# Kernel optimization log

Hardware: AMD Instinct MI355X
Metric: run time of the kernel (lower is better)

## Reference

```python
import jax, jax.numpy as jnp
import numpy as np
import math

# Mamba2Simple(d_model=192, d_state=128, d_conv=4, expand=4, headdim=32, chunk_size=256)
D_MODEL = 192
D_STATE = 128
D_CONV = 4
EXPAND = 4
HEADDIM = 32
D_INNER = EXPAND * D_MODEL                      # 768
NHEADS = D_INNER // HEADDIM                     # 24
CONV_DIM = D_INNER + 2 * D_STATE                # 1024 (ngroups=1)
D_IN_PROJ = 2 * D_INNER + 2 * D_STATE + NHEADS  # 1816
SEQ_PAD = 256                                   # forward pads dim-2 to 256
NUM_CLASS = 100
FEATURE_DIM = HEADDIM * D_STATE                 # 4096, classifier input


def make_pe(max_len, d_model):
    # TemporalPositionalEncoding buffer (sin/cos), added over the T axis.
    position = np.arange(max_len)[:, None].astype(np.float32)
    div_term = np.exp(np.arange(0, d_model, 2).astype(np.float32) * -(math.log(10000.0) / d_model))
    pe = np.zeros((max_len, d_model), np.float32)
    pe[:, 0::2] = np.sin(position * div_term)
    pe[:, 1::2] = np.cos(position * div_term)
    return jnp.asarray(pe)  # (max_len, d_model)


def setup_inputs() -> dict:
    key = jax.random.key(0)
    ks = jax.random.split(key, 8)
    B, T, S, D = 16, 8, 129, D_MODEL
    inputs = jax.random.normal(ks[0], (B, T, S, D), jnp.float32)
    in_proj_w = jax.random.normal(ks[1], (D_IN_PROJ, D_MODEL), jnp.float32) / np.sqrt(D_MODEL)
    conv_w = jax.random.normal(ks[2], (CONV_DIM, D_CONV), jnp.float32) / np.sqrt(D_CONV)
    conv_b = jax.random.normal(ks[3], (CONV_DIM,), jnp.float32) * 0.1
    # dt_bias = softplus^{-1}(dt) with dt ~ U[1e-3, 0.1] (Mamba2 init convention)
    dt0 = jax.random.uniform(ks[4], (NHEADS,), jnp.float32, 1e-3, 0.1)
    dt_bias = jnp.log(jnp.expm1(dt0))
    A_log = jnp.log(jax.random.uniform(ks[5], (NHEADS,), jnp.float32, 1.0, 16.0))
    cls_w = jax.random.normal(ks[6], (NUM_CLASS, FEATURE_DIM), jnp.float32) / np.sqrt(FEATURE_DIM)
    cls_b = jnp.zeros((NUM_CLASS,), jnp.float32)
    return dict(inputs=inputs, in_proj_w=in_proj_w, conv_w=conv_w, conv_b=conv_b,
                dt_bias=dt_bias, A_log=A_log, cls_w=cls_w, cls_b=cls_b)


def _mamba_final_state(u, in_proj_w, conv_w, conv_b, dt_bias, A_log):
    # u: (B, L, D_MODEL). Only the SSM final state is consumed downstream
    # (the module does `_, final_state = self.mamba(...)`), so the z / C / D /
    # RMSNormGated / out_proj branches, which never touch the state, are skipped.
    B_, L, _ = u.shape
    W = in_proj_w[D_INNER:, :]                              # rows for xBC (1024) + dt (24)
    proj = jnp.einsum('bld,ed->ble', u, W)                  # (B, L, 1048)
    xBC, dt_raw = proj[..., :CONV_DIM], proj[..., CONV_DIM:]
    # causal depthwise conv1d (kernel D_CONV) + SiLU
    xpad = jnp.pad(xBC, ((0, 0), (D_CONV - 1, 0), (0, 0)))
    conv = conv_b + sum(xpad[:, k:k + L, :] * conv_w[:, k] for k in range(D_CONV))
    xBC = jax.nn.silu(conv)
    x = xBC[..., :D_INNER].reshape(B_, L, NHEADS, HEADDIM)  # (B, L, H, P)
    Bmat = xBC[..., D_INNER:D_INNER + D_STATE]              # (B, L, N), ngroups=1
    dt = jax.nn.softplus(dt_raw + dt_bias)                  # (B, L, H)
    A = -jnp.exp(A_log)                                     # (H,), negative
    # Recurrence: h_t = exp(dt_t*A) * h_{t-1} + dt_t * x_t (outer) B_t.
    # Final state in closed form via exclusive suffix products of exp(dt*A):
    logdA = dt * A                                          # (B, L, H), <= 0
    csum = jnp.cumsum(logdA, axis=1)
    suffix = jnp.exp(csum[:, -1:, :] - csum)                # prod_{s>t} exp(dt_s*A)
    w = suffix * dt                                         # (B, L, H)
    return jnp.einsum('blh,blhp,bln->bhpn', w, x, Bmat)     # (B, H, P, N)


def reference(inputs, in_proj_w, conv_w, conv_b, dt_bias, A_log, cls_w, cls_b):
    # Dropout layers are identity in eval mode.
    B_, T, S, D = inputs.shape
    x = inputs[:, :, 1:, :]                                 # drop first sub-seq element
    pad = SEQ_PAD - x.shape[2]
    if pad > 0:
        x = jnp.pad(x, ((0, 0), (0, 0), (0, pad), (0, 0)))
    pe = make_pe(T, D)
    x = x + pe[None, :, None, :]                            # pe broadcast over batch & sub-seq
    preds = []
    for t in range(T):                                      # module re-runs scan on each suffix
        xt = x[:, t:, :, :].reshape(B_, -1, D)              # (B, (T-t)*256, D)
        h = _mamba_final_state(xt, in_proj_w, conv_w, conv_b, dt_bias, A_log)
        agg = h.sum(axis=1).reshape(B_, FEATURE_DIM)        # sum over heads -> (B, P*N)
        preds.append(agg @ cls_w.T + cls_b)
    return jnp.stack(preds, axis=1)                         # (B, T, NUM_CLASS)
```

## Files before the change

### kernel.cpp

```cpp
#include <hip/hip_runtime.h>
#include <math.h>

#define BATCH 16
#define TWIN 8
#define SEQIN 129
#define DMODEL 192
#define GLEN 2048
#define NH 24
#define HD 32
#define DS 128
#define NCC 896
#define MTOT (BATCH*GLEN)
#define NVALID (BATCH*TWIN*128)
#define PADK 40

typedef __attribute__((ext_vector_type(8))) short bf16x8;
typedef __attribute__((ext_vector_type(4))) float f32x4;

__device__ __forceinline__ float softplus_f(float x){
  return x > 20.f ? x : log1pf(expf(x));
}
__device__ __forceinline__ float silu_f(float x){
  return x / (1.f + __expf(-x));
}
__device__ __forceinline__ unsigned short tobf16(float f){
  union { float f; unsigned u; } v; v.f = f;
  unsigned r = v.u + 0x7FFF + ((v.u >> 16) & 1);
  return (unsigned short)(r >> 16);
}
__device__ __forceinline__ float frombf16(unsigned short u){
  union { unsigned u; float f; } v; v.u = ((unsigned)u) << 16; return v.f;
}
__device__ __forceinline__ bf16x8 pack8(float4 a, float4 b){
  bf16x8 r;
  r[0]=(short)tobf16(a.x); r[1]=(short)tobf16(a.y);
  r[2]=(short)tobf16(a.z); r[3]=(short)tobf16(a.w);
  r[4]=(short)tobf16(b.x); r[5]=(short)tobf16(b.y);
  r[6]=(short)tobf16(b.z); r[7]=(short)tobf16(b.w);
  return r;
}

__global__ __launch_bounds__(256) void k_build(const float* __restrict__ in,
    const float* __restrict__ inw, unsigned short* __restrict__ inh,
    unsigned short* __restrict__ wh, float* __restrict__ ptab,
    float* __restrict__ dtraw){
  __shared__ float smem[2048];
  int bx = blockIdx.x;
  int tid = threadIdx.x;
  if (bx < 768){
    int idx = (bx*256 + tid)*16;
    int v = idx / DMODEL;
    int d = idx - v*DMODEL;
    int bt = v >> 7, s = v & 127;
    const float* src = in + ((size_t)bt*SEQIN + s + 1)*DMODEL + d;
    float4 a0 = *(const float4*)src;
    float4 a1 = *(const float4*)(src+4);
    float4 a2 = *(const float4*)(src+8);
    float4 a3 = *(const float4*)(src+12);
    *(bf16x8*)&inh[idx]   = pack8(a0, a1);
    *(bf16x8*)&inh[idx+8] = pack8(a2, a3);
  } else if (bx < 852){
    int idx = ((bx-768)*256 + tid)*8;
    const float* src = inw + (size_t)768*DMODEL + idx;
    float4 a = *(const float4*)src;
    float4 b = *(const float4*)(src+4);
    *(bf16x8*)&wh[idx] = pack8(a, b);
  } else if (bx < 916){
    float* pe = smem;
    int pb = bx - 852;
    int t = pb >> 3, eslice = pb & 7;
    if (tid < DMODEL){
      int d = tid;
      float div = expf(-(float)(d & ~1) * (logf(10000.f)/(float)DMODEL));
      float ang = (float)t * div;
      pe[d] = (d & 1) ? cosf(ang) : sinf(ang);
    }
    __syncthreads();
    int e0 = eslice*115;
    int e1 = min(920, e0 + 115);
    for (int e = e0 + tid; e < e1; e += 256){
      int row = (e < 896) ? (768 + e) : (1792 + (e - 896));
      const float* wr = inw + (size_t)row*DMODEL;
      float s = 0.f;
      #pragma unroll 4
      for (int d = 0; d < DMODEL; d++)
        s += pe[d] * wr[d];
      ptab[t*920 + e] = s;
    }
  } else {
    float* As = smem;
    float* Bs = smem + 1024;
    int idx = bx - 916;
    int m0 = idx*64;
    int bt = m0 >> 7, srow = m0 & 127;
    int ty = tid >> 4, tx = tid & 15;
    int lr = tid >> 2, lq = tid & 3;
    float acc[4][4] = {};
    for (int k0 = 0; k0 < DMODEL; k0 += 16){
      float4 av = *(const float4*)(in + ((size_t)bt*SEQIN + srow + 1 + lr)*DMODEL + k0 + lq*4);
      As[(lq*4+0)*64+lr] = av.x; As[(lq*4+1)*64+lr] = av.y;
      As[(lq*4+2)*64+lr] = av.z; As[(lq*4+3)*64+lr] = av.w;
      float4 bv = make_float4(0.f,0.f,0.f,0.f);
      if (lr < NH) bv = *(const float4*)(inw + (size_t)(1792+lr)*DMODEL + k0 + lq*4);
      Bs[(lq*4+0)*64+lr] = bv.x; Bs[(lq*4+1)*64+lr] = bv.y;
      Bs[(lq*4+2)*64+lr] = bv.z; Bs[(lq*4+3)*64+lr] = bv.w;
      __syncthreads();
      #pragma unroll
      for (int kk = 0; kk < 16; kk++){
        float4 a = *(const float4*)&As[kk*64 + ty*4];
        float4 bq = *(const float4*)&Bs[kk*64 + tx*4];
        float avr[4] = {a.x, a.y, a.z, a.w};
        float bvr[4] = {bq.x, bq.y, bq.z, bq.w};
        #pragma unroll
        for (int i=0;i<4;i++)
          #pragma unroll
          for (int j=0;j<4;j++)
            acc[i][j] += avr[i]*bvr[j];
      }
      __syncthreads();
    }
    #pragma unroll
    for (int i=0;i<4;i++){
      int m = m0 + ty*4 + i;
      #pragma unroll
      for (int j=0;j<4;j++){
        int n = tx*4 + j;
        if (n < NH) dtraw[(size_t)m*NH + n] = acc[i][j];
      }
    }
  }
}

__global__ __launch_bounds__(256) void k_gemmall(const unsigned short* __restrict__ inh,
    const unsigned short* __restrict__ wh, const float* __restrict__ ptab,
    const float* __restrict__ dtraw, const float* __restrict__ dt_bias,
    const float* __restrict__ A_log, unsigned short* __restrict__ projh,
    float* __restrict__ wbuf, float* __restrict__ wsum){
  __shared__ char smem[20480];
  int bx = blockIdx.x;
  int tid = threadIdx.x;
  if (bx < 896){
    unsigned short* As = (unsigned short*)smem;
    unsigned short* Bs = As + 128*PADK;
    int mt = bx & 127;
    int n0 = (bx >> 7)*128;
    int t = mt & 7;
    size_t msrc = (size_t)mt*128;
    size_t mdst = (size_t)(mt >> 3)*GLEN + (size_t)t*256;
    int wid = tid >> 6, lane = tid & 63;
    int wm = (wid >> 1)*64, wn = (wid & 1)*64;
    int quad = lane >> 4, lm = lane & 15;
    int sr = tid >> 2, sq = tid & 3;
    f32x4 acc[4][4];
    #pragma unroll
    for (int i=0;i<4;i++)
      #pragma unroll
      for (int j=0;j<4;j++) acc[i][j] = (f32x4){0.f,0.f,0.f,0.f};
    for (int k0 = 0; k0 < DMODEL; k0 += 32){
      #pragma unroll
      for (int half=0; half<2; half++){
        int r = sr + half*64;
        *(bf16x8*)&As[r*PADK + sq*8] =
          *(const bf16x8*)&inh[(msrc + r)*DMODEL + k0 + sq*8];
        *(bf16x8*)&Bs[r*PADK + sq*8] =
          *(const bf16x8*)&wh[(size_t)(n0+r)*DMODEL + k0 + sq*8];
      }
      __syncthreads();
      bf16x8 aF[4], bF[4];
      #pragma unroll
      for (int i=0;i<4;i++){
        aF[i] = *(const bf16x8*)&As[(wm + i*16 + lm)*PADK + quad*8];
        bF[i] = *(const bf16x8*)&Bs[(wn + i*16 + lm)*PADK + quad*8];
      }
      #pragma unroll
      for (int i=0;i<4;i++)
        #pragma unroll
        for (int j=0;j<4;j++)
          acc[i][j] = __builtin_amdgcn_mfma_f32_16x16x32_bf16(aF[i], bF[j], acc[i][j], 0,0,0);
      __syncthreads();
    }
    float ptn[4];
    #pragma unroll
    for (int j=0;j<4;j++) ptn[j] = ptab[t*920 + n0 + wn + lm + j*16];
    #pragma unroll
    for (int i=0;i<4;i++){
      #pragma unroll
      for (int r=0;r<4;r++){
        int m = wm + i*16 + quad*4 + r;
        unsigned short* dst = projh + (mdst + m)*NCC + n0 + wn + lm;
        #pragma unroll
        for (int j=0;j<4;j++)
          dst[j*16] = tobf16(acc[i][j][r] + ptn[j]);
      }
    }
  } else if (bx < 1024){
    float* pt = (float*)smem;
    int bt = bx - 896;
    int b = bt >> 3, t = bt & 7;
    for (int e = tid; e < NCC; e += 256) pt[e] = ptab[t*920 + e];
    __syncthreads();
    size_t base = (size_t)b*GLEN + t*256;
    for (int i = tid; i < 12*224; i += 256){
      int r = i / 224, c4 = (i - r*224)*4;
      int s = (r < 8) ? (128 + r) : (244 + r);
      ushort4 v;
      v.x = tobf16(pt[c4+0]); v.y = tobf16(pt[c4+1]);
      v.z = tobf16(pt[c4+2]); v.w = tobf16(pt[c4+3]);
      *(ushort4*)&projh[(base + s)*NCC + c4] = v;
    }
  } else {
    float* wtot = (float*)smem;
    float* sred = (float*)smem + 4;
    int idx = bx - 1024;
    int h = idx % NH, b = idx / NH;
    int lane = tid & 63, wid = tid >> 6;
    int tw = tid >> 5, q = tid & 31;
    float dtb = dt_bias[h];
    float negA = -expf(A_log[h]);
    float off = ptab[tw*920 + 896 + h] + dtb;
    float dtv[8], pre[8];
    float run = 0.f;
    if (q < 16){
      size_t rb = ((size_t)(b*TWIN + tw)*128 + q*8)*NH + h;
      #pragma unroll
      for (int i=0;i<8;i++){
        float dt = softplus_f(dtraw[rb + (size_t)i*NH] + off);
        run += dt * negA;
        dtv[i] = dt; pre[i] = run;
      }
    } else {
      float dt = softplus_f(off);
      #pragma unroll
      for (int i=0;i<8;i++){
        run += dt * negA;
        dtv[i] = dt; pre[i] = run;
      }
    }
    float v = run;
    #pragma unroll
    for (int o=1; o<64; o<<=1){
      float u = __shfl_up(v, o, 64);
      if (lane >= o) v += u;
    }
    if (lane == 63) wtot[wid] = v;
    __syncthreads();
    float base = 0.f, total = 0.f;
    #pragma unroll
    for (int w2=0; w2<4; w2++){
      float tv = wtot[w2];
      if (w2 < wid) base += tv;
      total += tv;
    }
    float excl = base + v - run;
    float ls = 0.f;
    size_t gb = (size_t)b*GLEN + tw*256 + q*8;
    #pragma unroll
    for (int i=0;i<8;i++){
      float w = expf(total - (excl + pre[i])) * dtv[i];
      if (q < 17) wbuf[(gb + i)*NH + h] = w;
      else ls += w;
    }
    sred[tid] = ls;
    __syncthreads();
    if (q == 17){
      float acc = ls;
      for (int r = 18; r < 32; r++) acc += sred[tw*32 + r];
      wsum[((size_t)b*TWIN + tw)*NH + h] = acc;
    }
  }
}

__global__ __launch_bounds__(256) void k_foldall(const unsigned short* __restrict__ projh,
    const float* __restrict__ conv_w, const float* __restrict__ conv_b,
    const float* __restrict__ wbuf, const float* __restrict__ ptab,
    const float* __restrict__ wsum, float* __restrict__ partial,
    float* __restrict__ cB, float* __restrict__ cbuf){
  __shared__ float smem[5440];
  int bx = blockIdx.x;
  int tid = threadIdx.x;
  if (bx < 512){
    int bt = bx >> 2, sub = bx & 3;
    int b = bt >> 3, t = bt & 7;
    int wave = tid >> 6, lane = tid & 63;
    int g0 = t*256 + sub*34;
    int wstart = wave*8 + (wave > 0 ? 1 : 0);
    int gw = g0 + wstart;
    size_t rbase = (size_t)b*GLEN;
    float* ybuf = smem;
    float cb[7][2], cw[7][2][4];
    #pragma unroll
    for (int k=0;k<7;k++){
      int c = 2*lane + 128*k;
      float2 tb = *(const float2*)&conv_b[c];
      cb[k][0]=tb.x; cb[k][1]=tb.y;
      float4 w0 = *(const float4*)&conv_w[c*4];
      float4 w1 = *(const float4*)&conv_w[(c+1)*4];
      cw[k][0][0]=w0.x; cw[k][0][1]=w0.y; cw[k][0][2]=w0.z; cw[k][0][3]=w0.w;
      cw[k][1][0]=w1.x; cw[k][1][1]=w1.y; cw[k][1][2]=w1.z; cw[k][1][3]=w1.w;
    }
    float h0[7][2], h1[7][2], h2[7][2];
    #pragma unroll
    for (int k=0;k<7;k++){
      h0[k][0]=h0[k][1]=h1[k][0]=h1[k][1]=h2[k][0]=h2[k][1]=0.f;
    }
    if (gw >= 3){
      #pragma unroll
      for (int k=0;k<7;k++){
        int c = 2*lane + 128*k;
        ushort2 p0 = *(const ushort2*)&projh[(rbase+gw-3)*NCC + c];
        ushort2 p1 = *(const ushort2*)&projh[(rbase+gw-2)*NCC + c];
        ushort2 p2 = *(const ushort2*)&projh[(rbase+gw-1)*NCC + c];
        h0[k][0]=frombf16(p0.x); h0[k][1]=frombf16(p0.y);
        h1[k][0]=frombf16(p1.x); h1[k][1]=frombf16(p1.y);
        h2[k][0]=frombf16(p2.x); h2[k][1]=frombf16(p2.y);
      }
    }
    #pragma unroll
    for (int i=0;i<9;i++){
      size_t row = rbase + gw + i;
      float wreg = (lane < NH) ? wbuf[row*NH + lane] : 0.f;
      float cur[7][2];
      #pragma unroll
      for (int k=0;k<7;k++){
        int c = 2*lane + 128*k;
        ushort2 pv = *(const ushort2*)&projh[row*NCC + c];
        cur[k][0]=frombf16(pv.x); cur[k][1]=frombf16(pv.y);
      }
      float py0=0.f, py1=0.f, b0v=0.f, b1v=0.f;
      #pragma unroll
      for (int k=0;k<7;k++){
        float a0 = cb[k][0] + h0[k][0]*cw[k][0][0] + h1[k][0]*cw[k][0][1]
                            + h2[k][0]*cw[k][0][2] + cur[k][0]*cw[k][0][3];
        float a1 = cb[k][1] + h0[k][1]*cw[k][1][0] + h1[k][1]*cw[k][1][1]
                            + h2[k][1]*cw[k][1][2] + cur[k][1]*cw[k][1][3];
        float s0 = silu_f(a0), s1 = silu_f(a1);
        if (k < 6){
          float wh_ = __shfl(wreg, (lane>>4) + 4*k, 64);
          py0 += wh_*s0; py1 += wh_*s1;
        } else { b0v = s0; b1v = s1; }
      }
      py0 += __shfl_xor(py0, 16, 64); py0 += __shfl_xor(py0, 32, 64);
      py1 += __shfl_xor(py1, 16, 64); py1 += __shfl_xor(py1, 32, 64);
      float* dst = ybuf + (wstart + i)*160;
      if (lane < 16) *(float2*)&dst[2*lane] = make_float2(py0, py1);
      *(float2*)&dst[32 + 2*lane] = make_float2(b0v, b1v);
      #pragma unroll
      for (int k=0;k<7;k++){
        h0[k][0]=h1[k][0]; h0[k][1]=h1[k][1];
        h1[k][0]=h2[k][0]; h1[k][1]=h2[k][1];
        h2[k][0]=cur[k][0]; h2[k][1]=cur[k][1];
      }
    }
    __syncthreads();
    int p0 = (tid >> 5)*4, n0 = (tid & 31)*4;
    float acc[4][4] = {};
    #pragma unroll 2
    for (int gi = 0; gi < 34; gi++){
      float4 yv = *(const float4*)&ybuf[gi*160 + p0];
      float4 bv = *(const float4*)&ybuf[gi*160 + 32 + n0];
      float ya[4] = {yv.x,yv.y,yv.z,yv.w};
      float ba[4] = {bv.x,bv.y,bv.z,bv.w};
      #pragma unroll
      for (int i=0;i<4;i++)
        #pragma unroll
        for (int j=0;j<4;j++)
          acc[i][j] += ya[i]*ba[j];
    }
    size_t pb = ((size_t)bt*4 + sub)*4096;
    #pragma unroll
    for (int i=0;i<4;i++)
      #pragma unroll
      for (int j=0;j<4;j++)
        partial[pb + (p0+i)*128 + n0+j] = acc[i][j];
  } else if (bx < 640){
    float* Xc = smem;
    float* Ws = smem + 896;
    int idx = bx - 512;
    int t = idx & 7, b = idx >> 3;
    for (int c = tid; c < NCC; c += 256){
      float4 w = *(const float4*)&conv_w[c*4];
      float sw = w.x + w.y + w.z + w.w;
      float a = conv_b[c] + frombf16(tobf16(ptab[t*920 + c])) * sw;
      Xc[c] = silu_f(a);
    }
    if (tid < NH) Ws[tid] = wsum[((size_t)b*TWIN + t)*NH + tid];
    __syncthreads();
    float* dst = cB + ((size_t)(b*TWIN + t))*160;
    if (tid < 32){
      float y = 0.f;
      #pragma unroll
      for (int h=0;h<NH;h++) y += Ws[h]*Xc[h*32 + tid];
      dst[tid] = y;
    } else if (tid < 160){
      dst[tid] = Xc[768 + tid - 32];
    }
  } else {
    float* xsw  = smem;
    float* xsg  = smem + 896;
    float* wv   = smem + 1792;
    float* bufw = smem + 1816;
    float* bufg = smem + 2296;
    int idx = bx - 640;
    int b = idx / 7, t = idx % 7 + 1;
    size_t rbase = (size_t)b*GLEN;
    int g0 = t*256;
    for (int gi=0; gi<3; gi++){
      int g = g0 + gi;
      if (tid < NH) wv[tid] = wbuf[(rbase+g)*NH + tid];
      for (int c = tid; c < NCC; c += 256){
        float aw = conv_b[c], ag = conv_b[c];
        #pragma unroll
        for (int k=0;k<4;k++){
          int gp = g - 3 + k;
          float term = frombf16(projh[(rbase+gp)*NCC + c]) * conv_w[c*4+k];
          ag += term;
          if (gp >= g0) aw += term;
        }
        xsw[c] = silu_f(aw);
        xsg[c] = silu_f(ag);
      }
      __syncthreads();
      if (tid < 32){
        float yw = 0.f, yg = 0.f;
        #pragma unroll
        for (int h=0;h<NH;h++){ yw += wv[h]*xsw[h*32+tid]; yg += wv[h]*xsg[h*32+tid]; }
        bufw[gi*160 + tid] = yw;
        bufg[gi*160 + tid] = yg;
      } else if (tid < 160){
        bufw[gi*160 + tid] = xsw[768 + tid - 32];
        bufg[gi*160 + tid] = xsg[768 + tid - 32];
      }
      __syncthreads();
    }
    float* dst = cbuf + ((size_t)(b*TWIN + t))*960;
    for (int i = tid; i < 960; i += 256){
      int gi = i / 320, rem = i - gi*320;
      dst[i] = (rem < 160) ? bufw[gi*160 + rem] : bufg[gi*160 + rem - 160];
    }
  }
}

__global__ __launch_bounds__(256) void k_suffix(const float* __restrict__ partial,
    const float* __restrict__ cB, const float* __restrict__ cbuf,
    float* __restrict__ feat){
  int b = blockIdx.y;
  int e = blockIdx.x*256 + threadIdx.x;
  int p = e >> 7, n = e & 127;
  float s = 0.f;
  for (int t = TWIN-1; t >= 0; t--){
    int bt = b*TWIN + t;
    size_t pb = (size_t)bt*4*4096;
    s += partial[pb + e] + partial[pb + 4096 + e]
       + partial[pb + 2*4096 + e] + partial[pb + 3*4096 + e];
    const float* cb_ = cB + (size_t)bt*160;
    s += cb_[p] * cb_[32 + n];
    float f = s;
    if (t > 0){
      const float* cw_ = cbuf + (size_t)bt*960;
      #pragma unroll
      for (int gi=0; gi<3; gi++){
        const float* rw = cw_ + gi*320;
        f += rw[p]*rw[32+n] - rw[160+p]*rw[192+n];
      }
    }
    feat[(size_t)bt*4096 + e] = f;
  }
}

__global__ __launch_bounds__(256) void k_classifier(const float* __restrict__ feat,
    const float* __restrict__ cls_w, const float* __restrict__ cls_b,
    float* __restrict__ out){
  int bt0 = blockIdx.x*4;
  int k0  = blockIdx.y*4;
  int tid = threadIdx.x, wid = tid >> 6, lane = tid & 63;
  float acc[4][4] = {};
  int j0 = wid*1024;
  #pragma unroll
  for (int it = 0; it < 4; it++){
    int j = j0 + it*256 + lane*4;
    float4 f4[4], w4[4];
    #pragma unroll
    for (int i=0;i<4;i++) f4[i] = *(const float4*)(feat + (size_t)(bt0+i)*4096 + j);
    #pragma unroll
    for (int k=0;k<4;k++) w4[k] = *(const float4*)(cls_w + (size_t)(k0+k)*4096 + j);
    #pragma unroll
    for (int i=0;i<4;i++)
      #pragma unroll
      for (int k=0;k<4;k++)
        acc[i][k] += f4[i].x*w4[k].x + f4[i].y*w4[k].y
                   + f4[i].z*w4[k].z + f4[i].w*w4[k].w;
  }
  #pragma unroll
  for (int i=0;i<4;i++)
    #pragma unroll
    for (int k=0;k<4;k++)
      #pragma unroll
      for (int o=32; o>0; o>>=1)
        acc[i][k] += __shfl_down(acc[i][k], o, 64);
  __shared__ float part[4][16];
  if (lane == 0){
    #pragma unroll
    for (int i=0;i<4;i++)
      #pragma unroll
      for (int k=0;k<4;k++)
        part[wid][i*4+k] = acc[i][k];
  }
  __syncthreads();
  if (tid < 16){
    int i = tid >> 2, k = tid & 3;
    float s = part[0][tid] + part[1][tid] + part[2][tid] + part[3][tid];
    out[(size_t)(bt0+i)*100 + k0 + k] = s + cls_b[k0+k];
  }
}

extern "C" void kernel_launch(void* const* d_in, const int* in_sizes, int n_in,
                              void* d_out, int out_size, void* d_ws, size_t ws_size,
                              hipStream_t stream){
  const float* inputs    = (const float*)d_in[0];
  const float* in_proj_w = (const float*)d_in[1];
  const float* conv_w    = (const float*)d_in[2];
  const float* conv_b    = (const float*)d_in[3];
  const float* dt_bias   = (const float*)d_in[4];
  const float* A_log     = (const float*)d_in[5];
  const float* cls_w     = (const float*)d_in[6];
  const float* cls_b     = (const float*)d_in[7];
  float* out = (float*)d_out;

  unsigned short* projh= (unsigned short*)d_ws;
  float* dtraw         = (float*)(projh + (size_t)MTOT*NCC);
  float* wbuf          = dtraw + (size_t)NVALID*NH;
  unsigned short* inh  = (unsigned short*)(wbuf + (size_t)MTOT*NH);
  unsigned short* wh   = inh + (size_t)NVALID*DMODEL;
  float* partial       = (float*)(wh + (size_t)NCC*DMODEL);
  float* feat          = partial + (size_t)512*4096;
  float* ptab          = feat + (size_t)128*4096;
  float* wsum          = ptab + (size_t)8*920;
  float* cB            = wsum + (size_t)128*NH;
  float* cbuf          = cB + (size_t)128*160;
  size_t need = (size_t)((char*)(cbuf + (size_t)128*960) - (char*)d_ws);
  if (ws_size < need) return;

  k_build      <<<1172, 256, 0, stream>>>(inputs, in_proj_w, inh, wh, ptab, dtraw);
  k_gemmall    <<<1408, 256, 0, stream>>>(inh, wh, ptab, dtraw, dt_bias, A_log,
                                          projh, wbuf, wsum);
  k_foldall    <<<752, 256, 0, stream>>>(projh, conv_w, conv_b, wbuf, ptab, wsum,
                                         partial, cB, cbuf);
  k_suffix     <<<dim3(16, BATCH), 256, 0, stream>>>(partial, cB, cbuf, feat);
  k_classifier <<<dim3(32, 25), 256, 0, stream>>>(feat, cls_w, cls_b, out);
}
```

Measured before the change: 151.6 us.

## Deepen GEMM K-tile, fold pad-row fill into GEMM blocks, widen classifier tiles

The projection GEMM now stages 96-wide K slices in LDS instead of 32, which cuts the number of barrier pairs per tile at the cost of more shared memory per block and possibly lower occupancy. The separate pad-row fill blocks are removed. Each GEMM block now writes only 8 bias rows per tile, and the conv stages rebuild the pad-row values from ptab instead of reading them from projh. The classifier computes 8 classes per block with clamped loads, which halves its grid.

```diff
diff --git a/kernel.cpp b/kernel.cpp
--- a/kernel.cpp
+++ b/kernel.cpp
@@ -12,7 +12,7 @@
 #define NCC 896
 #define MTOT (BATCH*GLEN)
 #define NVALID (BATCH*TWIN*128)
-#define PADK 40
+#define PADK 104
 
 typedef __attribute__((ext_vector_type(8))) short bf16x8;
 typedef __attribute__((ext_vector_type(4))) float f32x4;
@@ -136,7 +136,7 @@
     const float* __restrict__ dtraw, const float* __restrict__ dt_bias,
     const float* __restrict__ A_log, unsigned short* __restrict__ projh,
     float* __restrict__ wbuf, float* __restrict__ wsum){
-  __shared__ char smem[20480];
+  __shared__ char smem[53248];
   int bx = blockIdx.x;
   int tid = threadIdx.x;
   if (bx < 896){
@@ -156,27 +156,33 @@
     for (int i=0;i<4;i++)
       #pragma unroll
       for (int j=0;j<4;j++) acc[i][j] = (f32x4){0.f,0.f,0.f,0.f};
-    for (int k0 = 0; k0 < DMODEL; k0 += 32){
-      #pragma unroll
-      for (int half=0; half<2; half++){
-        int r = sr + half*64;
-        *(bf16x8*)&As[r*PADK + sq*8] =
-          *(const bf16x8*)&inh[(msrc + r)*DMODEL + k0 + sq*8];
-        *(bf16x8*)&Bs[r*PADK + sq*8] =
-          *(const bf16x8*)&wh[(size_t)(n0+r)*DMODEL + k0 + sq*8];
+    for (int k0 = 0; k0 < DMODEL; k0 += 96){
+      #pragma unroll
+      for (int kk = 0; kk < 96; kk += 32){
+        #pragma unroll
+        for (int half=0; half<2; half++){
+          int r = sr + half*64;
+          *(bf16x8*)&As[r*PADK + kk + sq*8] =
+            *(const bf16x8*)&inh[(msrc + r)*DMODEL + k0 + kk + sq*8];
+          *(bf16x8*)&Bs[r*PADK + kk + sq*8] =
+            *(const bf16x8*)&wh[(size_t)(n0+r)*DMODEL + k0 + kk + sq*8];
+        }
       }
       __syncthreads();
-      bf16x8 aF[4], bF[4];
-      #pragma unroll
-      for (int i=0;i<4;i++){
-        aF[i] = *(const bf16x8*)&As[(wm + i*16 + lm)*PADK + quad*8];
-        bF[i] = *(const bf16x8*)&Bs[(wn + i*16 + lm)*PADK + quad*8];
-      }
-      #pragma unroll
-      for (int i=0;i<4;i++)
-        #pragma unroll
-        for (int j=0;j<4;j++)
-          acc[i][j] = __builtin_amdgcn_mfma_f32_16x16x32_bf16(aF[i], bF[j], acc[i][j], 0,0,0);
+      #pragma unroll
+      for (int kk = 0; kk < 3; kk++){
+        bf16x8 aF[4], bF[4];
+        #pragma unroll
+        for (int i=0;i<4;i++){
+          aF[i] = *(const bf16x8*)&As[(wm + i*16 + lm)*PADK + kk*32 + quad*8];
+          bF[i] = *(const bf16x8*)&Bs[(wn + i*16 + lm)*PADK + kk*32 + quad*8];
+        }
+        #pragma unroll
+        for (int i=0;i<4;i++)
+          #pragma unroll
+          for (int j=0;j<4;j++)
+            acc[i][j] = __builtin_amdgcn_mfma_f32_16x16x32_bf16(aF[i], bF[j], acc[i][j], 0,0,0);
+      }
       __syncthreads();
     }
     float ptn[4];
@@ -193,25 +199,19 @@
           dst[j*16] = tobf16(acc[i][j][r] + ptn[j]);
       }
     }
-  } else if (bx < 1024){
-    float* pt = (float*)smem;
-    int bt = bx - 896;
-    int b = bt >> 3, t = bt & 7;
-    for (int e = tid; e < NCC; e += 256) pt[e] = ptab[t*920 + e];
-    __syncthreads();
-    size_t base = (size_t)b*GLEN + t*256;
-    for (int i = tid; i < 12*224; i += 256){
-      int r = i / 224, c4 = (i - r*224)*4;
-      int s = (r < 8) ? (128 + r) : (244 + r);
+    {
+      int r = tid >> 5;
+      int c4 = (tid & 31)*4;
+      float4 pv = *(const float4*)&ptab[t*920 + n0 + c4];
       ushort4 v;
-      v.x = tobf16(pt[c4+0]); v.y = tobf16(pt[c4+1]);
-      v.z = tobf16(pt[c4+2]); v.w = tobf16(pt[c4+3]);
-      *(ushort4*)&projh[(base + s)*NCC + c4] = v;
+      v.x = tobf16(pv.x); v.y = tobf16(pv.y);
+      v.z = tobf16(pv.z); v.w = tobf16(pv.w);
+      *(ushort4*)&projh[(mdst + 128 + r)*NCC + n0 + c4] = v;
     }
   } else {
     float* wtot = (float*)smem;
     float* sred = (float*)smem + 4;
-    int idx = bx - 1024;
+    int idx = bx - 896;
     int h = idx % NH, b = idx / NH;
     int lane = tid & 63, wid = tid >> 6;
     int tw = tid >> 5, q = tid & 31;
@@ -304,15 +304,28 @@
       h0[k][0]=h0[k][1]=h1[k][0]=h1[k][1]=h2[k][0]=h2[k][1]=0.f;
     }
     if (gw >= 3){
-      #pragma unroll
-      for (int k=0;k<7;k++){
-        int c = 2*lane + 128*k;
-        ushort2 p0 = *(const ushort2*)&projh[(rbase+gw-3)*NCC + c];
-        ushort2 p1 = *(const ushort2*)&projh[(rbase+gw-2)*NCC + c];
-        ushort2 p2 = *(const ushort2*)&projh[(rbase+gw-1)*NCC + c];
-        h0[k][0]=frombf16(p0.x); h0[k][1]=frombf16(p0.y);
-        h1[k][0]=frombf16(p1.x); h1[k][1]=frombf16(p1.y);
-        h2[k][0]=frombf16(p2.x); h2[k][1]=frombf16(p2.y);
+      if ((gw & 255) == 0){
+        int tp = (gw >> 8) - 1;
+        #pragma unroll
+        for (int k=0;k<7;k++){
+          int c = 2*lane + 128*k;
+          float v0 = frombf16(tobf16(ptab[tp*920 + c]));
+          float v1 = frombf16(tobf16(ptab[tp*920 + c + 1]));
+          h0[k][0]=v0; h0[k][1]=v1;
+          h1[k][0]=v0; h1[k][1]=v1;
+          h2[k][0]=v0; h2[k][1]=v1;
+        }
+      } else {
+        #pragma unroll
+        for (int k=0;k<7;k++){
+          int c = 2*lane + 128*k;
+          ushort2 p0 = *(const ushort2*)&projh[(rbase+gw-3)*NCC + c];
+          ushort2 p1 = *(const ushort2*)&projh[(rbase+gw-2)*NCC + c];
+          ushort2 p2 = *(const ushort2*)&projh[(rbase+gw-1)*NCC + c];
+          h0[k][0]=frombf16(p0.x); h0[k][1]=frombf16(p0.y);
+          h1[k][0]=frombf16(p1.x); h1[k][1]=frombf16(p1.y);
+          h2[k][0]=frombf16(p2.x); h2[k][1]=frombf16(p2.y);
+        }
       }
     }
     #pragma unroll
@@ -412,7 +425,9 @@
         #pragma unroll
         for (int k=0;k<4;k++){
           int gp = g - 3 + k;
-          float term = frombf16(projh[(rbase+gp)*NCC + c]) * conv_w[c*4+k];
+          float pj = (gp >= g0) ? frombf16(projh[(rbase+gp)*NCC + c])
+                                : frombf16(tobf16(ptab[(t-1)*920 + c]));
+          float term = pj * conv_w[c*4+k];
           ag += term;
           if (gp >= g0) aw += term;
         }
@@ -471,45 +486,49 @@
     const float* __restrict__ cls_w, const float* __restrict__ cls_b,
     float* __restrict__ out){
   int bt0 = blockIdx.x*4;
-  int k0  = blockIdx.y*4;
+  int k0  = blockIdx.y*8;
   int tid = threadIdx.x, wid = tid >> 6, lane = tid & 63;
-  float acc[4][4] = {};
+  float acc[4][8] = {};
   int j0 = wid*1024;
   #pragma unroll
   for (int it = 0; it < 4; it++){
     int j = j0 + it*256 + lane*4;
-    float4 f4[4], w4[4];
+    float4 f4[4], w4[8];
     #pragma unroll
     for (int i=0;i<4;i++) f4[i] = *(const float4*)(feat + (size_t)(bt0+i)*4096 + j);
     #pragma unroll
-    for (int k=0;k<4;k++) w4[k] = *(const float4*)(cls_w + (size_t)(k0+k)*4096 + j);
+    for (int k=0;k<8;k++){
+      int kr = k0 + k; kr = kr < 100 ? kr : 99;
+      w4[k] = *(const float4*)(cls_w + (size_t)kr*4096 + j);
+    }
     #pragma unroll
     for (int i=0;i<4;i++)
       #pragma unroll
-      for (int k=0;k<4;k++)
+      for (int k=0;k<8;k++)
         acc[i][k] += f4[i].x*w4[k].x + f4[i].y*w4[k].y
                    + f4[i].z*w4[k].z + f4[i].w*w4[k].w;
   }
   #pragma unroll
   for (int i=0;i<4;i++)
     #pragma unroll
-    for (int k=0;k<4;k++)
+    for (int k=0;k<8;k++)
       #pragma unroll
       for (int o=32; o>0; o>>=1)
         acc[i][k] += __shfl_down(acc[i][k], o, 64);
-  __shared__ float part[4][16];
+  __shared__ float part[4][32];
   if (lane == 0){
     #pragma unroll
     for (int i=0;i<4;i++)
       #pragma unroll
-      for (int k=0;k<4;k++)
-        part[wid][i*4+k] = acc[i][k];
+      for (int k=0;k<8;k++)
+        part[wid][i*8+k] = acc[i][k];
   }
   __syncthreads();
-  if (tid < 16){
-    int i = tid >> 2, k = tid & 3;
+  if (tid < 32){
+    int i = tid >> 3, k = tid & 7;
     float s = part[0][tid] + part[1][tid] + part[2][tid] + part[3][tid];
-    out[(size_t)(bt0+i)*100 + k0 + k] = s + cls_b[k0+k];
+    int kr = k0 + k;
+    if (kr < 100) out[(size_t)(bt0+i)*100 + kr] = s + cls_b[kr];
   }
 }
 
@@ -541,10 +560,10 @@
   if (ws_size < need) return;
 
   k_build      <<<1172, 256, 0, stream>>>(inputs, in_proj_w, inh, wh, ptab, dtraw);
-  k_gemmall    <<<1408, 256, 0, stream>>>(inh, wh, ptab, dtraw, dt_bias, A_log,
+  k_gemmall    <<<1280, 256, 0, stream>>>(inh, wh, ptab, dtraw, dt_bias, A_log,
                                           projh, wbuf, wsum);
   k_foldall    <<<752, 256, 0, stream>>>(projh, conv_w, conv_b, wbuf, ptab, wsum,
                                          partial, cB, cbuf);
   k_suffix     <<<dim3(16, BATCH), 256, 0, stream>>>(partial, cB, cbuf, feat);
-  k_classifier <<<dim3(32, 25), 256, 0, stream>>>(feat, cls_w, cls_b, out);
-}
+  k_classifier <<<dim3(32, 13), 256, 0, stream>>>(feat, cls_w, cls_b, out);
+}
```

After: 153.3 us. Within noise of the previous version (+1.2%).
